# Performance work log

Measured on AMD Instinct MI355X. Metric: run time of the kernel, lower is better.

Reference implementation:

```python
import jax, jax.numpy as jnp
import numpy as np

N = 100000   # nodes
E = 1600000  # edges
F_IN = 128
HID = 128
C = 40
EPS = 1e-5


def setup_inputs() -> dict:
    key = jax.random.key(0)
    ks = jax.random.split(key, 8)
    x = jax.random.normal(ks[0], (N, F_IN), dtype=jnp.float32)
    edge_index = jax.random.randint(ks[1], (2, E), 0, N, dtype=jnp.int32)
    s = 0.05
    return {
        "x": x,
        "edge_index": edge_index,
        "W1": jax.random.normal(ks[2], (F_IN, HID), dtype=jnp.float32) * s,
        "b1": jnp.zeros((HID,), jnp.float32),
        "g1": jnp.ones((HID,), jnp.float32),
        "be1": jnp.zeros((HID,), jnp.float32),
        "W2": jax.random.normal(ks[3], (HID, HID), dtype=jnp.float32) * s,
        "b2": jnp.zeros((HID,), jnp.float32),
        "g2": jnp.ones((HID,), jnp.float32),
        "be2": jnp.zeros((HID,), jnp.float32),
        "W3": jax.random.normal(ks[4], (HID, C), dtype=jnp.float32) * s,
        "b3": jnp.zeros((C,), jnp.float32),
    }


def _gcn_conv(x, W, b, src, dst, deg_inv_sqrt):
    # h = X W; then symmetric-normalized aggregation over edges (incl. self loops)
    h = x @ W                                  # [N, out]
    coef = deg_inv_sqrt[src] * deg_inv_sqrt[dst]  # [E+N]
    msg = h[src] * coef[:, None]               # gather + scale
    out = jax.ops.segment_sum(msg, dst, num_segments=N)
    return out + b


def _batchnorm(x, g, be):
    mean = jnp.mean(x, axis=0)
    var = jnp.mean(jnp.square(x - mean), axis=0)  # biased var (torch BN train)
    return (x - mean) * jax.lax.rsqrt(var + EPS) * g + be


def reference(x, edge_index, W1, b1, g1, be1, W2, b2, g2, be2, W3, b3):
    # add self loops once
    loop = jnp.arange(N, dtype=edge_index.dtype)
    src = jnp.concatenate([edge_index[0], loop])
    dst = jnp.concatenate([edge_index[1], loop])
    deg = jax.ops.segment_sum(jnp.ones_like(dst, dtype=x.dtype), dst, num_segments=N)
    dinv = jax.lax.rsqrt(deg)  # deg >= 1 due to self loops

    h = _gcn_conv(x, W1, b1, src, dst, dinv)
    h = _batchnorm(h, g1, be1)
    h = h + x                      # residual: hidden_dim == num_features
    h = jax.nn.relu(h)             # dropout: eval-mode identity

    h = _gcn_conv(h, W2, b2, src, dst, dinv)
    h = _batchnorm(h, g2, be2)
    h = jax.nn.relu(h)

    h = _gcn_conv(h, W3, b3, src, dst, dinv)
    return jax.nn.log_softmax(h, axis=1)
```

## Files before the change

### kernel.cpp

```cpp
#include <hip/hip_runtime.h>
#include <hip/hip_bf16.h>

#define NN 100000
#define EE 1600000
#define HID 128
#define CLS 40
#define EPSBN 1e-5f
#define NBUK ((NN + 255) >> 8)
#define CAP 6144
#define EPB 4096
#define NPB 512

typedef float f32x4 __attribute__((ext_vector_type(4)));
typedef float f32x2 __attribute__((ext_vector_type(2)));
typedef short s16x8 __attribute__((ext_vector_type(8)));
union U48 { uint4 u; s16x8 s; };

static __device__ __forceinline__ unsigned short f2bf(float f) {
    unsigned u = __float_as_uint(f);
    unsigned r = (u + 0x7fff + ((u >> 16) & 1)) >> 16;
    return (unsigned short)r;
}
static __device__ __forceinline__ unsigned pack2(float a, float b) {
    return (unsigned)f2bf(a) | ((unsigned)f2bf(b) << 16);
}
static __device__ __forceinline__ float bflo(unsigned v) { return __uint_as_float(v << 16); }
static __device__ __forceinline__ float bfhi(unsigned v) { return __uint_as_float(v & 0xffff0000u); }


__global__ void prep_all(const float* __restrict__ W1, const float* __restrict__ W2,
                         const float* __restrict__ W3,
                         unsigned* __restrict__ Wf1, unsigned* __restrict__ Wf2,
                         unsigned* __restrict__ Wf3,
                         int* gcur, float* stats1, float* stats2) {
    int blk = blockIdx.x;
    int tid = threadIdx.x;
    if (blk < 64) {
        const float* W = (blk < 32) ? W1 : W2;
        unsigned* Wf = (blk < 32) ? Wf1 : Wf2;
        int t = ((blk & 31) << 8) + tid;
        int q = t & 3, lane = (t >> 2) & 63, f = t >> 8;
        int ks = f >> 3, ct = f & 7;
        int k = ks * 32 + ((lane >> 4) << 3) + q * 2;
        int col = ct * 16 + (lane & 15);
        Wf[t] = pack2(W[k * 128 + col], W[(k + 1) * 128 + col]);
    } else if (blk < 76) {
        int t = ((blk - 64) << 8) + tid;
        int q = t & 3, lane = (t >> 2) & 63, f = t >> 8;
        int ks = f / 3, ct = f - ks * 3;
        int k = ks * 32 + ((lane >> 4) << 3) + q * 2;
        int col = ct * 16 + (lane & 15);
        float v0 = (col < CLS) ? W3[k * CLS + col] : 0.0f;
        float v1 = (col < CLS) ? W3[(k + 1) * CLS + col] : 0.0f;
        Wf3[t] = pack2(v0, v1);
    } else {
        int j = ((blk - 76) << 8) + tid;
        if (j < NBUK) gcur[j] = j * CAP;
        if (blk == 76) {
            stats1[tid] = 0.0f;
            stats2[tid] = 0.0f;
        }
    }
}


__global__ __launch_bounds__(256) void fill_p1_binned(const int* __restrict__ src,
                                                      const int* __restrict__ dst,
                                                      int* gcur, int* __restrict__ tmp) {
    __shared__ int cnt[NBUK];
    __shared__ int base[NBUK];
    int tid = threadIdx.x;
    for (int j = tid; j < NBUK; j += 256) cnt[j] = 0;
    __syncthreads();

    int es[16], ed[16];
    int i0 = blockIdx.x * EPB;
#pragma unroll
    for (int k = 0; k < 16; k++) {
        int i = i0 + k * 256 + tid;
        bool ok = i < EE;
        es[k] = ok ? src[i] : -1;
        ed[k] = ok ? dst[i] : 0;
        if (ok) atomicAdd(&cnt[ed[k] >> 8], 1);
    }
    __syncthreads();
    for (int j = tid; j < NBUK; j += 256) {
        int c = cnt[j];
        base[j] = c ? atomicAdd(&gcur[j], c) : 0;
        cnt[j] = 0;
    }
    __syncthreads();
#pragma unroll
    for (int k = 0; k < 16; k++) {
        if (es[k] >= 0) {
            int b = ed[k] >> 8;
            int r = atomicAdd(&cnt[b], 1);
            tmp[base[b] + r] = (es[k] << 8) | (ed[k] & 255);
        }
    }
}

__global__ __launch_bounds__(512) void bucket_scan(const int* __restrict__ gcur,
                                                   int* __restrict__ gbase,
                                                   int* __restrict__ row_ptr) {
    __shared__ int sc[512];
    int tid = threadIdx.x;
    int v = (tid < NBUK) ? gcur[tid] - tid * CAP : 0;
    sc[tid] = v;
    __syncthreads();
    for (int off = 1; off < 512; off <<= 1) {
        int t = (tid >= off) ? sc[tid - off] : 0;
        __syncthreads();
        sc[tid] += t;
        __syncthreads();
    }
    if (tid < NBUK) gbase[tid] = sc[tid] - v;
    if (tid == NBUK - 1) {
        gbase[NBUK] = sc[tid];
        row_ptr[NN] = sc[tid];
    }
}

__global__ __launch_bounds__(256) void fill_p2(const int* __restrict__ tmp,
                                               const int* __restrict__ gcur,
                                               const int* __restrict__ gbase,
                                               float* __restrict__ dinv,
                                               int* __restrict__ row_ptr,
                                               int* __restrict__ csr) {
    __shared__ int cnt[256];
    __shared__ int sc[256];
    __shared__ int cur[256];
    int b = blockIdx.x;
    int tid = threadIdx.x;
    int total = gcur[b] - b * CAP;
    cnt[tid] = 0;
    __syncthreads();
    int lo = b * CAP;
    for (int k = tid; k < total; k += 256) atomicAdd(&cnt[tmp[lo + k] & 255], 1);
    __syncthreads();
    int c = cnt[tid];
    sc[tid] = c;
    __syncthreads();
    for (int off = 1; off < 256; off <<= 1) {
        int t = (tid >= off) ? sc[tid - off] : 0;
        __syncthreads();
        sc[tid] += t;
        __syncthreads();
    }
    int node = (b << 8) + tid;
    int rp = gbase[b] + sc[tid] - c;
    if (node < NN) {
        dinv[node] = rsqrtf((float)(c + 1));
        row_ptr[node] = rp;
    }
    cur[tid] = rp;
    __syncthreads();
    for (int k = tid; k < total; k += 256) {
        int v = tmp[lo + k];
        int p = atomicAdd(&cur[v & 255], 1);
        csr[p] = ((unsigned)v) >> 8;
    }
}


#define LDA 136

template <int MODE>
__global__ __launch_bounds__(256) void gemm128_mfma(const float* __restrict__ Xf,
                                                    const unsigned* __restrict__ Xb,
                                                    const unsigned* __restrict__ Wf,
                                                    const float* __restrict__ stats,
                                                    const float* __restrict__ gam,
                                                    const float* __restrict__ bet,
                                                    const float* __restrict__ xres,
                                                    const float* __restrict__ dinv,
                                                    unsigned char* __restrict__ Hb) {
    __shared__ unsigned short As[64 * LDA];
    __shared__ float scs[128];
    __shared__ float shs[128];
    int t = threadIdx.x;
    int lane = t & 63, w = t >> 6;
    int wr = w >> 1, wc = w & 1;
    int blk_row = blockIdx.x * 64;
    const float invN = 1.0f / (float)NN;

    s16x8 b[4][4];
    const uint4* Wv = (const uint4*)Wf;
#pragma unroll
    for (int ks = 0; ks < 4; ks++)
#pragma unroll
        for (int ct = 0; ct < 4; ct++) {
            int f = ks * 8 + wc * 4 + ct;
            U48 u; u.u = Wv[f * 64 + lane];
            b[ks][ct] = u.s;
        }

    if (MODE == 1) {
        if (t < 128) {
            float mean = stats[t] * invN;
            float var = stats[128 + t] * invN - mean * mean;
            float sc = gam[t] * rsqrtf(var + EPSBN);
            scs[t] = sc;
            shs[t] = bet[t] - mean * sc;
        }
        __syncthreads();
        const uint2* H2 = (const uint2*)Xb;
        const float4* R4 = (const float4*)xres;
#pragma unroll
        for (int i = 0; i < 8; i++) {
            int idx = i * 256 + t;
            int row = idx >> 5, c4 = idx & 31;
            int grow = blk_row + row;
            uint2 h = make_uint2(0u, 0u);
            float4 r = make_float4(0, 0, 0, 0);
            if (grow < NN) {
                h = H2[(size_t)grow * 32 + c4];
                r = R4[(size_t)grow * 32 + c4];
            }
            int f0 = c4 * 4;
            float v0 = fmaxf(fmaf(bflo(h.x), scs[f0 + 0], shs[f0 + 0]) + r.x, 0.0f);
            float v1 = fmaxf(fmaf(bfhi(h.x), scs[f0 + 1], shs[f0 + 1]) + r.y, 0.0f);
            float v2 = fmaxf(fmaf(bflo(h.y), scs[f0 + 2], shs[f0 + 2]) + r.z, 0.0f);
            float v3 = fmaxf(fmaf(bfhi(h.y), scs[f0 + 3], shs[f0 + 3]) + r.w, 0.0f);
            *(uint2*)&As[row * LDA + c4 * 4] = make_uint2(pack2(v0, v1), pack2(v2, v3));
        }
    } else {
        const float4* X4 = (const float4*)Xf;
#pragma unroll
        for (int i = 0; i < 8; i++) {
            int idx = i * 256 + t;
            int row = idx >> 5, c4 = idx & 31;
            int grow = blk_row + row;
            float4 a = make_float4(0, 0, 0, 0);
            if (grow < NN) a = X4[(size_t)grow * 32 + c4];
            *(uint2*)&As[row * LDA + c4 * 4] = make_uint2(pack2(a.x, a.y), pack2(a.z, a.w));
        }
    }
    __syncthreads();

    f32x4 acc[2][4] = {};
    int lrow = lane & 15;
    int koff = (lane >> 4) << 3;

#pragma unroll
    for (int ks = 0; ks < 4; ks++) {
        int k0 = ks * 32 + koff;
#pragma unroll
        for (int rf = 0; rf < 2; rf++) {
            int rloc = wr * 32 + rf * 16 + lrow;
            U48 a;
            a.u = *(const uint4*)&As[rloc * LDA + k0];
#pragma unroll
            for (int ct = 0; ct < 4; ct++)
                acc[rf][ct] = __builtin_amdgcn_mfma_f32_16x16x32_bf16(a.s, b[ks][ct], acc[rf][ct], 0, 0, 0);
        }
    }

#pragma unroll
    for (int rf = 0; rf < 2; rf++) {
        int rbase = blk_row + wr * 32 + rf * 16 + ((lane >> 4) << 2);
        float dv[4];
#pragma unroll
        for (int r = 0; r < 4; r++) dv[r] = (rbase + r < NN) ? dinv[rbase + r] : 0.0f;
#pragma unroll
        for (int ct = 0; ct < 4; ct++) {
            int col = wc * 64 + ct * 16 + lrow;
#pragma unroll
            for (int r = 0; r < 4; r++) {
                int row = rbase + r;
                if (row < NN) {
                    int pv = __builtin_amdgcn_cvt_pk_fp8_f32(acc[rf][ct][r] * dv[r], 0.0f, 0, false);
                    Hb[(size_t)row * 128 + col] = (unsigned char)pv;
                }
            }
        }
    }
}

__global__ __launch_bounds__(256) void gemm40_mfma(const unsigned* __restrict__ Xb,
                                                   const unsigned* __restrict__ Wf,
                                                   const float* __restrict__ stats,
                                                   const float* __restrict__ gam,
                                                   const float* __restrict__ bet,
                                                   const float* __restrict__ dinv,
                                                   unsigned char* __restrict__ H3) {
    __shared__ unsigned short As[64 * LDA];
    __shared__ float scs[128];
    __shared__ float shs[128];
    int t = threadIdx.x;
    int lane = t & 63, w = t >> 6;
    int blk_row = blockIdx.x * 64;
    const float invN = 1.0f / (float)NN;

    s16x8 b[4][3];
    const uint4* Wv = (const uint4*)Wf;
#pragma unroll
    for (int ks = 0; ks < 4; ks++)
#pragma unroll
        for (int ct = 0; ct < 3; ct++) {
            U48 u; u.u = Wv[(ks * 3 + ct) * 64 + lane];
            b[ks][ct] = u.s;
        }

    if (t < 128) {
        float mean = stats[t] * invN;
        float var = stats[128 + t] * invN - mean * mean;
        float sc = gam[t] * rsqrtf(var + EPSBN);
        scs[t] = sc;
        shs[t] = bet[t] - mean * sc;
    }
    __syncthreads();
    const uint2* H2 = (const uint2*)Xb;
#pragma unroll
    for (int i = 0; i < 8; i++) {
        int idx = i * 256 + t;
        int row = idx >> 5, c4 = idx & 31;
        int grow = blk_row + row;
        uint2 h = make_uint2(0u, 0u);
        if (grow < NN) h = H2[(size_t)grow * 32 + c4];
        int f0 = c4 * 4;
        float v0 = fmaxf(fmaf(bflo(h.x), scs[f0 + 0], shs[f0 + 0]), 0.0f);
        float v1 = fmaxf(fmaf(bfhi(h.x), scs[f0 + 1], shs[f0 + 1]), 0.0f);
        float v2 = fmaxf(fmaf(bflo(h.y), scs[f0 + 2], shs[f0 + 2]), 0.0f);
        float v3 = fmaxf(fmaf(bfhi(h.y), scs[f0 + 3], shs[f0 + 3]), 0.0f);
        *(uint2*)&As[row * LDA + c4 * 4] = make_uint2(pack2(v0, v1), pack2(v2, v3));
    }
    __syncthreads();

    f32x4 acc[3] = {};
    int lrow = lane & 15;
    int koff = (lane >> 4) << 3;

#pragma unroll
    for (int ks = 0; ks < 4; ks++) {
        int k0 = ks * 32 + koff;
        int rloc = w * 16 + lrow;
        U48 a;
        a.u = *(const uint4*)&As[rloc * LDA + k0];
#pragma unroll
        for (int ct = 0; ct < 3; ct++)
            acc[ct] = __builtin_amdgcn_mfma_f32_16x16x32_bf16(a.s, b[ks][ct], acc[ct], 0, 0, 0);
    }

    int rbase = blk_row + w * 16 + ((lane >> 4) << 2);
    float dv[4];
#pragma unroll
    for (int r = 0; r < 4; r++) dv[r] = (rbase + r < NN) ? dinv[rbase + r] : 0.0f;
#pragma unroll
    for (int ct = 0; ct < 3; ct++) {
        int col = ct * 16 + lrow;
        if (col >= CLS) continue;
#pragma unroll
        for (int r = 0; r < 4; r++) {
            int row = rbase + r;
            if (row < NN) {
                int pv = __builtin_amdgcn_cvt_pk_fp8_f32(acc[ct][r] * dv[r], 0.0f, 0, false);
                H3[(size_t)row * CLS + col] = (unsigned char)pv;
            }
        }
    }
}


__global__ __launch_bounds__(256) void agg128_half(const unsigned* __restrict__ h8,
                                                   const int* __restrict__ row_ptr,
                                                   const int* __restrict__ csr,
                                                   const float* __restrict__ dinv,
                                                   const float* __restrict__ bias,
                                                   uint2* __restrict__ outb) {
    int wid = threadIdx.x >> 6;
    int lane = threadIdx.x & 63;
    int half = lane >> 5, l = lane & 31;
    int node = blockIdx.x * 8 + wid * 2 + half;

    unsigned sv = h8[(size_t)node * 32 + l];
    f32x2 alo = __builtin_amdgcn_cvt_pk_f32_fp8(sv, false);
    f32x2 ahi = __builtin_amdgcn_cvt_pk_f32_fp8(sv, true);

    int beg = row_ptr[node], end = row_ptr[node + 1];
    int cnt = end - beg;
    int cmax = max(cnt, __shfl_xor(cnt, 32));

    for (int k = 0; k < cmax; k += 12) {
        int si[12];
        unsigned g[12];
#pragma unroll
        for (int j = 0; j < 12; j++) {
            int idx = beg + k + j;
            si[j] = csr[(idx < end) ? idx : beg];
        }
#pragma unroll
        for (int j = 0; j < 12; j++) {
            int idx = beg + k + j;
            g[j] = (idx < end) ? h8[(size_t)si[j] * 32 + l] : 0u;
        }
#pragma unroll
        for (int j = 0; j < 12; j++) {
            alo += __builtin_amdgcn_cvt_pk_f32_fp8(g[j], false);
            ahi += __builtin_amdgcn_cvt_pk_f32_fp8(g[j], true);
        }
    }

    float di = dinv[node];
    float4 b = *(const float4*)&bias[l * 4];
    outb[(size_t)node * 32 + l] =
        make_uint2(pack2(fmaf(alo.x, di, b.x), fmaf(alo.y, di, b.y)),
                   pack2(fmaf(ahi.x, di, b.z), fmaf(ahi.y, di, b.w)));
}

__global__ __launch_bounds__(256) void agg40_lsm(const unsigned* __restrict__ h3,
                                                 const int* __restrict__ row_ptr,
                                                 const int* __restrict__ csr,
                                                 const float* __restrict__ dinv,
                                                 const float* __restrict__ b3,
                                                 float* __restrict__ out) {
    int wid = threadIdx.x >> 6;
    int lane = threadIdx.x & 63;
    int half = lane >> 5, l30 = lane & 31;
    int slot = l30 / 10;
    int fp = l30 - slot * 10;
    bool sok = slot < 3;
    int node = blockIdx.x * 8 + wid * 2 + half;

    f32x2 alo = {0.0f, 0.0f}, ahi = {0.0f, 0.0f};
    if (slot == 0) {
        unsigned v = h3[(size_t)node * 10 + fp];
        alo = __builtin_amdgcn_cvt_pk_f32_fp8(v, false);
        ahi = __builtin_amdgcn_cvt_pk_f32_fp8(v, true);
    }
    int beg = row_ptr[node], end = row_ptr[node + 1];
    int cnt = end - beg;
    for (int k = 0; k < cnt; k += 12) {
#pragma unroll
        for (int jj = 0; jj < 4; jj++) {
            int idx = beg + k + jj * 3 + slot;
            bool on = sok && (idx < end);
            int s = csr[on ? idx : beg];
            unsigned g = on ? h3[(size_t)s * 10 + fp] : 0u;
            alo += __builtin_amdgcn_cvt_pk_f32_fp8(g, false);
            ahi += __builtin_amdgcn_cvt_pk_f32_fp8(g, true);
        }
    }
    float a0 = alo.x, a1 = alo.y, a2 = ahi.x, a3 = ahi.y;
    float t0 = __shfl(a0, lane + 10), t1 = __shfl(a1, lane + 10);
    float t2 = __shfl(a2, lane + 10), t3 = __shfl(a3, lane + 10);
    float u0 = __shfl(a0, lane + 20), u1 = __shfl(a1, lane + 20);
    float u2 = __shfl(a2, lane + 20), u3 = __shfl(a3, lane + 20);
    bool fin = l30 < 10;
    float l0 = 0.0f, l1 = 0.0f, l2 = 0.0f, l3 = 0.0f;
    if (fin) {
        float di = dinv[node];
        float4 b = *(const float4*)&b3[fp * 4];
        l0 = fmaf(a0 + t0 + u0, di, b.x);
        l1 = fmaf(a1 + t1 + u1, di, b.y);
        l2 = fmaf(a2 + t2 + u2, di, b.z);
        l3 = fmaf(a3 + t3 + u3, di, b.w);
    }
    float m = fin ? fmaxf(fmaxf(l0, l1), fmaxf(l2, l3)) : -1e30f;
#pragma unroll
    for (int off = 16; off > 0; off >>= 1) m = fmaxf(m, __shfl_xor(m, off));
    float s = fin ? (expf(l0 - m) + expf(l1 - m) + expf(l2 - m) + expf(l3 - m)) : 0.0f;
#pragma unroll
    for (int off = 16; off > 0; off >>= 1) s += __shfl_xor(s, off);
    float lse = m + logf(s);
    if (fin)
        *(float4*)&out[(size_t)node * CLS + fp * 4] =
            make_float4(l0 - lse, l1 - lse, l2 - lse, l3 - lse);
}


__global__ __launch_bounds__(256) void bn_part(const uint2* __restrict__ a,
                                               float* __restrict__ gpart, int n) {
    __shared__ float red[4][256];
    int tid = threadIdx.x;
    int w = tid >> 6, lane = tid & 63;
    int half = lane >> 5, l = lane & 31;
    int gw = blockIdx.x * 4 + w;
    float s0 = 0.f, s1 = 0.f, s2 = 0.f, s3 = 0.f;
    float q0 = 0.f, q1 = 0.f, q2 = 0.f, q3 = 0.f;
    int npair = n >> 1;
    for (int p = gw; p < npair; p += NPB * 4) {
        int row = p * 2 + half;
        uint2 u = a[(size_t)row * 32 + l];
        float v0 = bflo(u.x), v1 = bfhi(u.x), v2 = bflo(u.y), v3 = bfhi(u.y);
        s0 += v0; q0 = fmaf(v0, v0, q0);
        s1 += v1; q1 = fmaf(v1, v1, q1);
        s2 += v2; q2 = fmaf(v2, v2, q2);
        s3 += v3; q3 = fmaf(v3, v3, q3);
    }
    s0 += __shfl_xor(s0, 32); s1 += __shfl_xor(s1, 32);
    s2 += __shfl_xor(s2, 32); s3 += __shfl_xor(s3, 32);
    q0 += __shfl_xor(q0, 32); q1 += __shfl_xor(q1, 32);
    q2 += __shfl_xor(q2, 32); q3 += __shfl_xor(q3, 32);
    if (half == 0) {
        red[w][l * 4 + 0] = s0; red[w][l * 4 + 1] = s1;
        red[w][l * 4 + 2] = s2; red[w][l * 4 + 3] = s3;
        red[w][128 + l * 4 + 0] = q0; red[w][128 + l * 4 + 1] = q1;
        red[w][128 + l * 4 + 2] = q2; red[w][128 + l * 4 + 3] = q3;
    }
    __syncthreads();
    float pv = red[0][tid] + red[1][tid] + red[2][tid] + red[3][tid];
    gpart[(size_t)blockIdx.x * 256 + tid] = pv;
}

__global__ __launch_bounds__(256) void bn_final(const float* __restrict__ gpart,
                                                float* __restrict__ stats) {
    int t = threadIdx.x;
    int k0 = blockIdx.x * (NPB / 8);
    float s = 0.0f;
#pragma unroll 8
    for (int k = k0; k < k0 + NPB / 8; k++)
        s += gpart[(size_t)k * 256 + t];
    atomicAdd(&stats[t], s);
}


extern "C" void kernel_launch(void* const* d_in, const int* in_sizes, int n_in,
                              void* d_out, int out_size, void* d_ws, size_t ws_size,
                              hipStream_t stream) {
    const float* x   = (const float*)d_in[0];
    const int*   ei  = (const int*)d_in[1];
    const float* W1  = (const float*)d_in[2];
    const float* b1  = (const float*)d_in[3];
    const float* g1  = (const float*)d_in[4];
    const float* be1 = (const float*)d_in[5];
    const float* W2  = (const float*)d_in[6];
    const float* b2  = (const float*)d_in[7];
    const float* g2  = (const float*)d_in[8];
    const float* be2 = (const float*)d_in[9];
    const float* W3  = (const float*)d_in[10];
    const float* b3  = (const float*)d_in[11];
    float* out = (float*)d_out;

    const int* src = ei;
    const int* dst = ei + EE;

    char* w = (char*)d_ws;
    size_t off = 0;
    auto alloc = [&](size_t bytes) {
        void* p = w + off;
        off += (bytes + 255) & ~(size_t)255;
        return p;
    };
    float* dinv      = (float*)alloc((size_t)NN * 4);
    int*   row_ptr   = (int*)alloc((size_t)(NN + 1) * 4);
    int*   gcur      = (int*)alloc((size_t)NBUK * 4);
    int*   gbase     = (int*)alloc((size_t)(NBUK + 1) * 4);
    int*   tmp       = (int*)alloc((size_t)NBUK * CAP * 4);
    int*   csr       = (int*)alloc((size_t)EE * 4);
    float* stats1    = (float*)alloc(256 * 4);
    float* stats2    = (float*)alloc(256 * 4);
    float* gpart     = (float*)alloc((size_t)NPB * 256 * 4);
    unsigned* Wf1    = (unsigned*)alloc(8192 * 4);
    unsigned* Wf2    = (unsigned*)alloc(8192 * 4);
    unsigned* Wf3    = (unsigned*)alloc(3072 * 4);
    unsigned* aH     = (unsigned*)alloc((size_t)NN * 64 * 4);
    unsigned char* hB8 = (unsigned char*)alloc((size_t)NN * 128);
    unsigned char* h3b = (unsigned char*)alloc((size_t)NN * 40);

    const int NB_P1 = (EE + EPB - 1) / EPB;
    const int NB_G  = (NN + 63) / 64;

    prep_all<<<78, 256, 0, stream>>>(W1, W2, W3, Wf1, Wf2, Wf3, gcur, stats1, stats2);
    fill_p1_binned<<<NB_P1, 256, 0, stream>>>(src, dst, gcur, tmp);
    bucket_scan<<<1, 512, 0, stream>>>(gcur, gbase, row_ptr);
    fill_p2<<<NBUK, 256, 0, stream>>>(tmp, gcur, gbase, dinv, row_ptr, csr);

    gemm128_mfma<0><<<NB_G, 256, 0, stream>>>(x, nullptr, Wf1, nullptr, nullptr, nullptr, nullptr, dinv, hB8);
    agg128_half<<<NN / 8, 256, 0, stream>>>((const unsigned*)hB8, row_ptr, csr, dinv, b1, (uint2*)aH);
    bn_part<<<NPB, 256, 0, stream>>>((const uint2*)aH, gpart, NN);
    bn_final<<<8, 256, 0, stream>>>(gpart, stats1);

    gemm128_mfma<1><<<NB_G, 256, 0, stream>>>(nullptr, aH, Wf2, stats1, g1, be1, x, dinv, hB8);
    agg128_half<<<NN / 8, 256, 0, stream>>>((const unsigned*)hB8, row_ptr, csr, dinv, b2, (uint2*)aH);
    bn_part<<<NPB, 256, 0, stream>>>((const uint2*)aH, gpart, NN);
    bn_final<<<8, 256, 0, stream>>>(gpart, stats2);

    gemm40_mfma<<<NB_G, 256, 0, stream>>>(aH, Wf3, stats2, g2, be2, dinv, h3b);
    agg40_lsm<<<NN / 8, 256, 0, stream>>>((const unsigned*)h3b, row_ptr, csr, dinv, b3, out);
}
```

Before: 267.8 us.

## Fuse BN partial statistics into aggregation and share CSR indices via shuffles

```diff
diff --git a/kernel.cpp b/kernel.cpp
--- a/kernel.cpp
+++ b/kernel.cpp
@@ -9,7 +9,7 @@
 #define NBUK ((NN + 255) >> 8)
 #define CAP 6144
 #define EPB 4096
-#define NPB 512
+#define GROWS (NN / 8)
 
 typedef float f32x4 __attribute__((ext_vector_type(4)));
 typedef float f32x2 __attribute__((ext_vector_type(2)));
@@ -367,9 +367,12 @@
                                                    const int* __restrict__ csr,
                                                    const float* __restrict__ dinv,
                                                    const float* __restrict__ bias,
-                                                   uint2* __restrict__ outb) {
-    int wid = threadIdx.x >> 6;
-    int lane = threadIdx.x & 63;
+                                                   uint2* __restrict__ outb,
+                                                   float* __restrict__ gpart) {
+    __shared__ float red[4][256];
+    int tid = threadIdx.x;
+    int wid = tid >> 6;
+    int lane = tid & 63;
     int half = lane >> 5, l = lane & 31;
     int node = blockIdx.x * 8 + wid * 2 + half;
 
@@ -380,19 +383,18 @@
     int beg = row_ptr[node], end = row_ptr[node + 1];
     int cnt = end - beg;
     int cmax = max(cnt, __shfl_xor(cnt, 32));
+    int hb = (lane & 32);
 
     for (int k = 0; k < cmax; k += 12) {
-        int si[12];
+        int bidx = beg + k + l;
+        int cl = (bidx < end) ? bidx : beg;
+        int myv = (l < 12) ? csr[cl] : 0;
         unsigned g[12];
 #pragma unroll
         for (int j = 0; j < 12; j++) {
+            int si = __shfl(myv, hb + j);
             int idx = beg + k + j;
-            si[j] = csr[(idx < end) ? idx : beg];
-        }
-#pragma unroll
-        for (int j = 0; j < 12; j++) {
-            int idx = beg + k + j;
-            g[j] = (idx < end) ? h8[(size_t)si[j] * 32 + l] : 0u;
+            g[j] = (idx < end) ? h8[(size_t)si * 32 + l] : 0u;
         }
 #pragma unroll
         for (int j = 0; j < 12; j++) {
@@ -403,9 +405,25 @@
 
     float di = dinv[node];
     float4 b = *(const float4*)&bias[l * 4];
-    outb[(size_t)node * 32 + l] =
-        make_uint2(pack2(fmaf(alo.x, di, b.x), fmaf(alo.y, di, b.y)),
-                   pack2(fmaf(ahi.x, di, b.z), fmaf(ahi.y, di, b.w)));
+    float o0 = fmaf(alo.x, di, b.x), o1 = fmaf(alo.y, di, b.y);
+    float o2 = fmaf(ahi.x, di, b.z), o3 = fmaf(ahi.y, di, b.w);
+    outb[(size_t)node * 32 + l] = make_uint2(pack2(o0, o1), pack2(o2, o3));
+
+    float s0 = o0, s1 = o1, s2 = o2, s3 = o3;
+    float q0 = o0 * o0, q1 = o1 * o1, q2 = o2 * o2, q3 = o3 * o3;
+    s0 += __shfl_xor(s0, 32); s1 += __shfl_xor(s1, 32);
+    s2 += __shfl_xor(s2, 32); s3 += __shfl_xor(s3, 32);
+    q0 += __shfl_xor(q0, 32); q1 += __shfl_xor(q1, 32);
+    q2 += __shfl_xor(q2, 32); q3 += __shfl_xor(q3, 32);
+    if (half == 0) {
+        red[wid][l * 4 + 0] = s0; red[wid][l * 4 + 1] = s1;
+        red[wid][l * 4 + 2] = s2; red[wid][l * 4 + 3] = s3;
+        red[wid][128 + l * 4 + 0] = q0; red[wid][128 + l * 4 + 1] = q1;
+        red[wid][128 + l * 4 + 2] = q2; red[wid][128 + l * 4 + 3] = q3;
+    }
+    __syncthreads();
+    float pv = red[0][tid] + red[1][tid] + red[2][tid] + red[3][tid];
+    gpart[(size_t)blockIdx.x * 256 + tid] = pv;
 }
 
 __global__ __launch_bounds__(256) void agg40_lsm(const unsigned* __restrict__ h3,
@@ -469,49 +487,15 @@
 }
 
 
-__global__ __launch_bounds__(256) void bn_part(const uint2* __restrict__ a,
-                                               float* __restrict__ gpart, int n) {
-    __shared__ float red[4][256];
-    int tid = threadIdx.x;
-    int w = tid >> 6, lane = tid & 63;
-    int half = lane >> 5, l = lane & 31;
-    int gw = blockIdx.x * 4 + w;
-    float s0 = 0.f, s1 = 0.f, s2 = 0.f, s3 = 0.f;
-    float q0 = 0.f, q1 = 0.f, q2 = 0.f, q3 = 0.f;
-    int npair = n >> 1;
-    for (int p = gw; p < npair; p += NPB * 4) {
-        int row = p * 2 + half;
-        uint2 u = a[(size_t)row * 32 + l];
-        float v0 = bflo(u.x), v1 = bfhi(u.x), v2 = bflo(u.y), v3 = bfhi(u.y);
-        s0 += v0; q0 = fmaf(v0, v0, q0);
-        s1 += v1; q1 = fmaf(v1, v1, q1);
-        s2 += v2; q2 = fmaf(v2, v2, q2);
-        s3 += v3; q3 = fmaf(v3, v3, q3);
-    }
-    s0 += __shfl_xor(s0, 32); s1 += __shfl_xor(s1, 32);
-    s2 += __shfl_xor(s2, 32); s3 += __shfl_xor(s3, 32);
-    q0 += __shfl_xor(q0, 32); q1 += __shfl_xor(q1, 32);
-    q2 += __shfl_xor(q2, 32); q3 += __shfl_xor(q3, 32);
-    if (half == 0) {
-        red[w][l * 4 + 0] = s0; red[w][l * 4 + 1] = s1;
-        red[w][l * 4 + 2] = s2; red[w][l * 4 + 3] = s3;
-        red[w][128 + l * 4 + 0] = q0; red[w][128 + l * 4 + 1] = q1;
-        red[w][128 + l * 4 + 2] = q2; red[w][128 + l * 4 + 3] = q3;
-    }
-    __syncthreads();
-    float pv = red[0][tid] + red[1][tid] + red[2][tid] + red[3][tid];
-    gpart[(size_t)blockIdx.x * 256 + tid] = pv;
-}
-
 __global__ __launch_bounds__(256) void bn_final(const float* __restrict__ gpart,
                                                 float* __restrict__ stats) {
     int t = threadIdx.x;
-    int k0 = blockIdx.x * (NPB / 8);
+    int k0 = blockIdx.x * 196;
+    int k1 = (k0 + 196 < GROWS) ? k0 + 196 : GROWS;
     float s = 0.0f;
-#pragma unroll 8
-    for (int k = k0; k < k0 + NPB / 8; k++)
+    for (int k = k0; k < k1; k++)
         s += gpart[(size_t)k * 256 + t];
-    atomicAdd(&stats[t], s);
+    if (k0 < GROWS) atomicAdd(&stats[t], s);
 }
 
 
@@ -550,7 +534,7 @@
     int*   csr       = (int*)alloc((size_t)EE * 4);
     float* stats1    = (float*)alloc(256 * 4);
     float* stats2    = (float*)alloc(256 * 4);
-    float* gpart     = (float*)alloc((size_t)NPB * 256 * 4);
+    float* gpart     = (float*)alloc((size_t)GROWS * 256 * 4);
     unsigned* Wf1    = (unsigned*)alloc(8192 * 4);
     unsigned* Wf2    = (unsigned*)alloc(8192 * 4);
     unsigned* Wf3    = (unsigned*)alloc(3072 * 4);
@@ -567,14 +551,12 @@
     fill_p2<<<NBUK, 256, 0, stream>>>(tmp, gcur, gbase, dinv, row_ptr, csr);
 
     gemm128_mfma<0><<<NB_G, 256, 0, stream>>>(x, nullptr, Wf1, nullptr, nullptr, nullptr, nullptr, dinv, hB8);
-    agg128_half<<<NN / 8, 256, 0, stream>>>((const unsigned*)hB8, row_ptr, csr, dinv, b1, (uint2*)aH);
-    bn_part<<<NPB, 256, 0, stream>>>((const uint2*)aH, gpart, NN);
-    bn_final<<<8, 256, 0, stream>>>(gpart, stats1);
+    agg128_half<<<NN / 8, 256, 0, stream>>>((const unsigned*)hB8, row_ptr, csr, dinv, b1, (uint2*)aH, gpart);
+    bn_final<<<64, 256, 0, stream>>>(gpart, stats1);
 
     gemm128_mfma<1><<<NB_G, 256, 0, stream>>>(nullptr, aH, Wf2, stats1, g1, be1, x, dinv, hB8);
-    agg128_half<<<NN / 8, 256, 0, stream>>>((const unsigned*)hB8, row_ptr, csr, dinv, b2, (uint2*)aH);
-    bn_part<<<NPB, 256, 0, stream>>>((const uint2*)aH, gpart, NN);
-    bn_final<<<8, 256, 0, stream>>>(gpart, stats2);
+    agg128_half<<<NN / 8, 256, 0, stream>>>((const unsigned*)hB8, row_ptr, csr, dinv, b2, (uint2*)aH, gpart);
+    bn_final<<<64, 256, 0, stream>>>(gpart, stats2);
 
     gemm40_mfma<<<NB_G, 256, 0, stream>>>(aH, Wf3, stats2, g2, be2, dinv, h3b);
     agg40_lsm<<<NN / 8, 256, 0, stream>>>((const unsigned*)h3b, row_ptr, csr, dinv, b3, out);
```

Result: slower. 331.2 us (+23.6%).
